# Kernel optimization log

Measured on AMD Instinct MI355X. Metric: run time of the kernel, lower is better.

## Reference

```python
import jax, jax.numpy as jnp
import numpy as np

N = 100000      # nodes
F_IN = 500      # input features
HEADS = 8
HID = 8         # per-head hidden channels
NC = 16         # num classes
E = 1600000     # edges (avg degree 16)


def setup_inputs() -> dict:
    key = jax.random.key(0)
    ks = jax.random.split(key, 12)
    s = 0.1
    return {
        "x": jax.random.normal(ks[0], (N, F_IN), jnp.float32),
        "edge_index": jax.random.randint(ks[1], (2, E), 0, N, dtype=jnp.int64),
        "W1": jax.random.normal(ks[2], (F_IN, HEADS * HID), jnp.float32) * s,
        "a1_src": jax.random.normal(ks[3], (HEADS, HID), jnp.float32) * s,
        "a1_dst": jax.random.normal(ks[4], (HEADS, HID), jnp.float32) * s,
        "b1": jnp.zeros((HEADS * HID,), jnp.float32),
        "W2": jax.random.normal(ks[5], (HEADS * HID, NC), jnp.float32) * s,
        "a2_src": jax.random.normal(ks[6], (1, NC), jnp.float32) * s,
        "a2_dst": jax.random.normal(ks[7], (1, NC), jnp.float32) * s,
        "b2": jnp.zeros((NC,), jnp.float32),
        "Wg": jax.random.normal(ks[8], (NC, NC), jnp.float32) * s,
        "bg": jnp.zeros((NC,), jnp.float32),
    }


def _gat_layer(x, src, dst, W, a_src, a_dst, b, heads, ch):
    # PyG GATConv (eval mode): per-edge additive attention + scatter softmax.
    n = x.shape[0]
    h = (x @ W).reshape(n, heads, ch)                       # [N,H,C]
    al_s = jnp.einsum('nhc,hc->nh', h, a_src)               # [N,H]
    al_d = jnp.einsum('nhc,hc->nh', h, a_dst)
    e = jax.nn.leaky_relu(al_s[src] + al_d[dst], 0.2)       # [Etot,H]
    e_max = jax.ops.segment_max(e, dst, num_segments=n)     # stable softmax per dst
    ex = jnp.exp(e - e_max[dst])
    denom = jax.ops.segment_sum(ex, dst, num_segments=n)
    alpha = ex / (denom[dst] + 1e-16)                       # [Etot,H]
    out = jax.ops.segment_sum(alpha[:, :, None] * h[src], dst, num_segments=n)
    return out.reshape(n, heads * ch) + b


def _gcn_layer(x, src, dst, W, b):
    n = x.shape[0]
    deg = jax.ops.segment_sum(jnp.ones_like(dst, x.dtype), dst, num_segments=n)
    dinv = jnp.where(deg > 0, jax.lax.rsqrt(deg), 0.0)
    norm = dinv[src] * dinv[dst]                            # [Etot]
    xw = x @ W
    return jax.ops.segment_sum(norm[:, None] * xw[src], dst, num_segments=n) + b


def reference(x, edge_index, W1, a1_src, a1_dst, b1, W2, a2_src, a2_dst, b2, Wg, bg):
    n = x.shape[0]
    loop = jnp.arange(n, dtype=edge_index.dtype)
    src = jnp.concatenate([edge_index[0], loop])            # add self-loops (PyG default)
    dst = jnp.concatenate([edge_index[1], loop])
    # GAT: dropout layers are eval-mode no-ops
    h = jax.nn.elu(_gat_layer(x, src, dst, W1, a1_src, a1_dst, b1, HEADS, HID))
    h = _gat_layer(h, src, dst, W2, a2_src, a2_dst, b2, 1, NC)
    h = jax.nn.relu(h)                                      # activate='relu'
    return _gcn_layer(h, src, dst, Wg, bg)
```

## Files before the change

kernel.cpp:

```cpp
#include <hip/hip_runtime.h>
#include <hip/hip_bf16.h>
#include <math.h>

#define NNODES 100000
#define F_IN   500
#define KPAD   512
#define HEADS  8
#define HID    8
#define NC     16

typedef __attribute__((ext_vector_type(8))) short bf16x8;
typedef __attribute__((ext_vector_type(4))) float f32x4;
typedef __attribute__((ext_vector_type(8))) unsigned short u16x8;

__device__ inline unsigned short f2bf_rne(float f) {
    unsigned u = __float_as_uint(f);
    u += 0x7FFF + ((u >> 16) & 1);
    return (unsigned short)(u >> 16);
}
__device__ inline float bf2f(unsigned short h) {
    return __uint_as_float(((unsigned)h) << 16);
}

__global__ void zero_int_kernel(int* __restrict__ p, int n) {
    int i = blockIdx.x * blockDim.x + threadIdx.x;
    if (i < n) p[i] = 0;
}

__global__ void deg_kernel(const int* __restrict__ ei_dst, int* __restrict__ deg,
                           int E, int N) {
    int e = blockIdx.x * blockDim.x + threadIdx.x;
    int tot = E + N;
    if (e >= tot) return;
    int d = (e < E) ? ei_dst[e] : (e - E);
    atomicAdd(&deg[d], 1);
}

__global__ void scan1_kernel(const int* __restrict__ deg, int* __restrict__ bsum, int n) {
    __shared__ int s[256];
    int i = blockIdx.x * 256 + threadIdx.x;
    s[threadIdx.x] = (i < n) ? deg[i] : 0;
    __syncthreads();
    for (int off = 128; off > 0; off >>= 1) {
        if (threadIdx.x < off) s[threadIdx.x] += s[threadIdx.x + off];
        __syncthreads();
    }
    if (threadIdx.x == 0) bsum[blockIdx.x] = s[0];
}

__global__ void scan2_kernel(const int* __restrict__ bsum, int* __restrict__ bexcl, int nb) {
    __shared__ int s[512];
    int t = threadIdx.x;
    int orig = (t < nb) ? bsum[t] : 0;
    s[t] = orig;
    __syncthreads();
    for (int off = 1; off < 512; off <<= 1) {
        int v = (t >= off) ? s[t - off] : 0;
        __syncthreads();
        s[t] += v;
        __syncthreads();
    }
    if (t < nb) bexcl[t] = s[t] - orig;
}

__global__ void scan3_kernel(const int* __restrict__ deg, const int* __restrict__ bexcl,
                             int* __restrict__ rowptr, int n) {
    __shared__ int s[256];
    int t = threadIdx.x;
    int i = blockIdx.x * 256 + t;
    int v = (i < n) ? deg[i] : 0;
    s[t] = v;
    __syncthreads();
    for (int off = 1; off < 256; off <<= 1) {
        int u = (t >= off) ? s[t - off] : 0;
        __syncthreads();
        s[t] += u;
        __syncthreads();
    }
    if (i < n) rowptr[i + 1] = bexcl[blockIdx.x] + s[t];
    if (i == 0) rowptr[0] = 0;
}

__global__ void fill_kernel(const int* __restrict__ ei_src, const int* __restrict__ ei_dst,
                            const int* __restrict__ rowptr, int* __restrict__ cursor,
                            int* __restrict__ col, int E, int N) {
    int e = blockIdx.x * blockDim.x + threadIdx.x;
    int tot = E + N;
    if (e >= tot) return;
    int s, d;
    if (e < E) { s = ei_src[e]; d = ei_dst[e]; }
    else       { s = e - E;     d = s; }
    int pos = atomicAdd(&cursor[d], 1);
    col[rowptr[d] + pos] = s;
}

__global__ void transposeW1_kernel(const float* __restrict__ W, float* __restrict__ Wt) {
    int i = blockIdx.x * blockDim.x + threadIdx.x;
    if (i >= 64 * KPAD) return;
    int c = i >> 9;
    int k = i & (KPAD - 1);
    Wt[i] = (k < F_IN) ? W[k * 64 + c] : 0.f;
}

#define BM  128
#define BK  32
#define LDT 40

__global__ __launch_bounds__(256) void gemm1_mfma_kernel(
        const float* __restrict__ x, const float* __restrict__ Wt,
        float* __restrict__ h, int n) {
    __shared__ unsigned short sAh[BM * LDT];
    __shared__ unsigned short sAl[BM * LDT];
    __shared__ unsigned short sBh[64 * LDT];
    __shared__ unsigned short sBl[64 * LDT];

    int t = threadIdx.x;
    int wave = t >> 6, lane = t & 63;
    int l15 = lane & 15, kgrp = lane >> 4;
    int row0 = blockIdx.x * BM;
    int wrow0 = wave * 32;

    int ar = t >> 1;
    int ak = (t & 1) * 16;
    int bc = t >> 2;
    int bk = (t & 3) * 8;

    f32x4 acc[2][4];
#pragma unroll
    for (int m = 0; m < 2; ++m)
#pragma unroll
        for (int nn = 0; nn < 4; ++nn)
            acc[m][nn] = (f32x4){0.f, 0.f, 0.f, 0.f};

    const int gr = row0 + ar;

    for (int k0 = 0; k0 < KPAD; k0 += BK) {
        float av[16];
        if (gr < n) {
            if (k0 + BK <= F_IN) {
                const float4* p = (const float4*)(x + (size_t)gr * F_IN + k0 + ak);
                float4 q0 = p[0], q1 = p[1], q2 = p[2], q3 = p[3];
                av[0]=q0.x; av[1]=q0.y; av[2]=q0.z; av[3]=q0.w;
                av[4]=q1.x; av[5]=q1.y; av[6]=q1.z; av[7]=q1.w;
                av[8]=q2.x; av[9]=q2.y; av[10]=q2.z; av[11]=q2.w;
                av[12]=q3.x; av[13]=q3.y; av[14]=q3.z; av[15]=q3.w;
            } else {
#pragma unroll
                for (int j = 0; j < 16; ++j) {
                    int kk = k0 + ak + j;
                    av[j] = (kk < F_IN) ? x[(size_t)gr * F_IN + kk] : 0.f;
                }
            }
        } else {
#pragma unroll
            for (int j = 0; j < 16; ++j) av[j] = 0.f;
        }
        u16x8 ah0, ah1, al0, al1;
#pragma unroll
        for (int j = 0; j < 8; ++j) {
            unsigned short hi = f2bf_rne(av[j]);
            ah0[j] = hi;
            al0[j] = f2bf_rne(av[j] - bf2f(hi));
        }
#pragma unroll
        for (int j = 0; j < 8; ++j) {
            unsigned short hi = f2bf_rne(av[8 + j]);
            ah1[j] = hi;
            al1[j] = f2bf_rne(av[8 + j] - bf2f(hi));
        }
        *(u16x8*)&sAh[ar * LDT + ak]     = ah0;
        *(u16x8*)&sAh[ar * LDT + ak + 8] = ah1;
        *(u16x8*)&sAl[ar * LDT + ak]     = al0;
        *(u16x8*)&sAl[ar * LDT + ak + 8] = al1;

        const float4* bp = (const float4*)(Wt + (size_t)bc * KPAD + k0 + bk);
        float4 w0 = bp[0], w1 = bp[1];
        float bv[8] = {w0.x, w0.y, w0.z, w0.w, w1.x, w1.y, w1.z, w1.w};
        u16x8 bh, bl;
#pragma unroll
        for (int j = 0; j < 8; ++j) {
            unsigned short hi = f2bf_rne(bv[j]);
            bh[j] = hi;
            bl[j] = f2bf_rne(bv[j] - bf2f(hi));
        }
        *(u16x8*)&sBh[bc * LDT + bk] = bh;
        *(u16x8*)&sBl[bc * LDT + bk] = bl;

        __syncthreads();

        bf16x8 aH[2], aL[2], bH[4], bL[4];
#pragma unroll
        for (int m = 0; m < 2; ++m) {
            int r = wrow0 + m * 16 + l15;
            aH[m] = *(const bf16x8*)&sAh[r * LDT + kgrp * 8];
            aL[m] = *(const bf16x8*)&sAl[r * LDT + kgrp * 8];
        }
#pragma unroll
        for (int nn = 0; nn < 4; ++nn) {
            int c = nn * 16 + l15;
            bH[nn] = *(const bf16x8*)&sBh[c * LDT + kgrp * 8];
            bL[nn] = *(const bf16x8*)&sBl[c * LDT + kgrp * 8];
        }
#pragma unroll
        for (int m = 0; m < 2; ++m)
#pragma unroll
            for (int nn = 0; nn < 4; ++nn) {
                acc[m][nn] = __builtin_amdgcn_mfma_f32_16x16x32_bf16(aH[m], bH[nn], acc[m][nn], 0, 0, 0);
                acc[m][nn] = __builtin_amdgcn_mfma_f32_16x16x32_bf16(aH[m], bL[nn], acc[m][nn], 0, 0, 0);
                acc[m][nn] = __builtin_amdgcn_mfma_f32_16x16x32_bf16(aL[m], bH[nn], acc[m][nn], 0, 0, 0);
            }
        __syncthreads();
    }

#pragma unroll
    for (int m = 0; m < 2; ++m) {
#pragma unroll
        for (int nn = 0; nn < 4; ++nn) {
#pragma unroll
            for (int r = 0; r < 4; ++r) {
                int row = row0 + wrow0 + m * 16 + kgrp * 4 + r;
                if (row < n)
                    h[(size_t)row * 64 + nn * 16 + l15] = acc[m][nn][r];
            }
        }
    }
}

__global__ void proj_al1_kernel(const float* __restrict__ h, const float* __restrict__ a1s,
                                const float* __restrict__ a1d, float* __restrict__ als,
                                float* __restrict__ ald, int n) {
    int nid = blockIdx.x * blockDim.x + threadIdx.x;
    if (nid >= n) return;
    const float* hp = h + (size_t)nid * 64;
#pragma unroll
    for (int hd = 0; hd < 8; ++hd) {
        float s = 0.f, d = 0.f;
#pragma unroll
        for (int c = 0; c < 8; ++c) {
            float hv = hp[hd * 8 + c];
            s += hv * a1s[hd * 8 + c];
            d += hv * a1d[hd * 8 + c];
        }
        als[nid * 8 + hd] = s;
        ald[nid * 8 + hd] = d;
    }
}

__global__ void gat1_edge_kernel(const int* __restrict__ rowptr, const int* __restrict__ col,
                                 const float* __restrict__ als, const float* __restrict__ ald,
                                 const float* __restrict__ h, const float* __restrict__ b1,
                                 float* __restrict__ out1, int n) {
    int tid = blockIdx.x * blockDim.x + threadIdx.x;
    int dst = tid >> 3, hd = tid & 7;
    if (dst >= n) return;
    int beg = rowptr[dst], end = rowptr[dst + 1];
    float ad = ald[dst * 8 + hd];
    float acc[8] = {};
    float den = 0.f;
    for (int j = beg; j < end; ++j) {
        int s = col[j];
        float e = als[s * 8 + hd] + ad;
        e = e > 0.f ? e : 0.2f * e;
        float w = expf(e);
        den += w;
        const float4* hp = reinterpret_cast<const float4*>(h + (size_t)s * 64 + hd * 8);
        float4 v0 = hp[0], v1 = hp[1];
        acc[0] += w * v0.x; acc[1] += w * v0.y; acc[2] += w * v0.z; acc[3] += w * v0.w;
        acc[4] += w * v1.x; acc[5] += w * v1.y; acc[6] += w * v1.z; acc[7] += w * v1.w;
    }
    float inv = 1.f / (den + 1e-16f);
#pragma unroll
    for (int c = 0; c < 8; ++c) {
        float v = acc[c] * inv + b1[hd * 8 + c];
        v = (v > 0.f) ? v : expm1f(v);
        out1[(size_t)dst * 64 + hd * 8 + c] = v;
    }
}

__global__ void proj2_kernel(const float* __restrict__ out1, const float* __restrict__ W2,
                             const float* __restrict__ a2s, const float* __restrict__ a2d,
                             float* __restrict__ h2, float* __restrict__ al2s,
                             float* __restrict__ al2d, int n) {
    int nid = blockIdx.x * blockDim.x + threadIdx.x;
    if (nid >= n) return;
    const float* op = out1 + (size_t)nid * 64;
    float acc[16] = {};
#pragma unroll 8
    for (int k = 0; k < 64; ++k) {
        float o = op[k];
#pragma unroll
        for (int c = 0; c < 16; ++c) acc[c] += o * W2[k * 16 + c];
    }
    float s = 0.f, d = 0.f;
#pragma unroll
    for (int c = 0; c < 16; ++c) {
        s += acc[c] * a2s[c];
        d += acc[c] * a2d[c];
        h2[(size_t)nid * 16 + c] = acc[c];
    }
    al2s[nid] = s;
    al2d[nid] = d;
}

__global__ void gat2_edge_kernel(const int* __restrict__ rowptr, const int* __restrict__ col,
                                 const float* __restrict__ al2s, const float* __restrict__ al2d,
                                 const float* __restrict__ h2, const float* __restrict__ b2,
                                 const float* __restrict__ Wg, float* __restrict__ xw,
                                 float* __restrict__ dinv, int n) {
    int dst = blockIdx.x * blockDim.x + threadIdx.x;
    if (dst >= n) return;
    int beg = rowptr[dst], end = rowptr[dst + 1];
    float ad = al2d[dst];
    float acc[16] = {};
    float den = 0.f;
    for (int j = beg; j < end; ++j) {
        int s = col[j];
        float e = al2s[s] + ad;
        e = e > 0.f ? e : 0.2f * e;
        float w = expf(e);
        den += w;
        const float4* hp = reinterpret_cast<const float4*>(h2 + (size_t)s * 16);
        float4 v0 = hp[0], v1 = hp[1], v2 = hp[2], v3 = hp[3];
        acc[0]  += w * v0.x; acc[1]  += w * v0.y; acc[2]  += w * v0.z; acc[3]  += w * v0.w;
        acc[4]  += w * v1.x; acc[5]  += w * v1.y; acc[6]  += w * v1.z; acc[7]  += w * v1.w;
        acc[8]  += w * v2.x; acc[9]  += w * v2.y; acc[10] += w * v2.z; acc[11] += w * v2.w;
        acc[12] += w * v3.x; acc[13] += w * v3.y; acc[14] += w * v3.z; acc[15] += w * v3.w;
    }
    float inv = 1.f / (den + 1e-16f);
    float r[16];
#pragma unroll
    for (int c = 0; c < 16; ++c) {
        float v = acc[c] * inv + b2[c];
        r[c] = (v > 0.f) ? v : 0.f;
    }
#pragma unroll
    for (int cp = 0; cp < 16; ++cp) {
        float s2 = 0.f;
#pragma unroll
        for (int c = 0; c < 16; ++c) s2 += r[c] * Wg[c * 16 + cp];
        xw[(size_t)dst * 16 + cp] = s2;
    }
    dinv[dst] = 1.f / sqrtf((float)(end - beg));
}

__global__ void gcn_kernel(const int* __restrict__ rowptr, const int* __restrict__ col,
                           const float* __restrict__ xw, const float* __restrict__ dinv,
                           const float* __restrict__ bg, float* __restrict__ out, int n) {
    int dst = blockIdx.x * blockDim.x + threadIdx.x;
    if (dst >= n) return;
    int beg = rowptr[dst], end = rowptr[dst + 1];
    float di = dinv[dst];
    float acc[16] = {};
    for (int j = beg; j < end; ++j) {
        int s = col[j];
        float nm = dinv[s] * di;
        const float4* xp = reinterpret_cast<const float4*>(xw + (size_t)s * 16);
        float4 v0 = xp[0], v1 = xp[1], v2 = xp[2], v3 = xp[3];
        acc[0]  += nm * v0.x; acc[1]  += nm * v0.y; acc[2]  += nm * v0.z; acc[3]  += nm * v0.w;
        acc[4]  += nm * v1.x; acc[5]  += nm * v1.y; acc[6]  += nm * v1.z; acc[7]  += nm * v1.w;
        acc[8]  += nm * v2.x; acc[9]  += nm * v2.y; acc[10] += nm * v2.z; acc[11] += nm * v2.w;
        acc[12] += nm * v3.x; acc[13] += nm * v3.y; acc[14] += nm * v3.z; acc[15] += nm * v3.w;
    }
#pragma unroll
    for (int c = 0; c < 16; ++c)
        out[(size_t)dst * 16 + c] = acc[c] + bg[c];
}

extern "C" void kernel_launch(void* const* d_in, const int* in_sizes, int n_in,
                              void* d_out, int out_size, void* d_ws, size_t ws_size,
                              hipStream_t stream) {
    const float* x    = (const float*)d_in[0];
    const int*   ei   = (const int*)d_in[1];
    const float* W1   = (const float*)d_in[2];
    const float* a1s  = (const float*)d_in[3];
    const float* a1d  = (const float*)d_in[4];
    const float* b1   = (const float*)d_in[5];
    const float* W2   = (const float*)d_in[6];
    const float* a2s  = (const float*)d_in[7];
    const float* a2d  = (const float*)d_in[8];
    const float* b2   = (const float*)d_in[9];
    const float* Wg   = (const float*)d_in[10];
    const float* bg   = (const float*)d_in[11];
    float* out = (float*)d_out;

    const int N = in_sizes[0] / F_IN;
    const int E = in_sizes[1] / 2;
    const int Etot = E + N;

    char* base = (char*)d_ws;
    size_t off = 0;
    auto alloc = [&](size_t bytes) -> char* {
        char* p = base + off;
        off = (off + bytes + 255) & ~(size_t)255;
        return p;
    };
    float* h    = (float*)alloc((size_t)N * 64 * 4);
    float* als  = (float*)alloc((size_t)N * 8 * 4);
    float* ald  = (float*)alloc((size_t)N * 8 * 4);
    float* out1 = (float*)alloc((size_t)N * 64 * 4);
    float* h2   = (float*)alloc((size_t)N * 16 * 4);
    float* al2s = (float*)alloc((size_t)N * 4);
    float* al2d = (float*)alloc((size_t)N * 4);
    float* xw   = (float*)alloc((size_t)N * 16 * 4);
    float* dinv = (float*)alloc((size_t)N * 4);
    int*   deg  = (int*)alloc((size_t)N * 4);
    int*   cur  = (int*)alloc((size_t)N * 4);
    int*   rowptr = (int*)alloc((size_t)(N + 1) * 4);
    int*   bsum = (int*)alloc(512 * 4);
    int*   bexcl= (int*)alloc(512 * 4);
    int*   col  = (int*)alloc((size_t)Etot * 4);
    float* Wt   = (float*)alloc((size_t)64 * KPAD * 4);

    const int* ei_src = ei;
    const int* ei_dst = ei + E;

    const int TB = 256;
    int nbN  = (N + TB - 1) / TB;
    int nbE  = (Etot + TB - 1) / TB;
    int nbG  = (N + BM - 1) / BM;
    int nbA  = (N * 8 + TB - 1) / TB;

    zero_int_kernel<<<nbN, TB, 0, stream>>>(deg, N);
    zero_int_kernel<<<nbN, TB, 0, stream>>>(cur, N);
    deg_kernel<<<nbE, TB, 0, stream>>>(ei_dst, deg, E, N);
    scan1_kernel<<<nbN, TB, 0, stream>>>(deg, bsum, N);
    scan2_kernel<<<1, 512, 0, stream>>>(bsum, bexcl, nbN);
    scan3_kernel<<<nbN, TB, 0, stream>>>(deg, bexcl, rowptr, N);
    fill_kernel<<<nbE, TB, 0, stream>>>(ei_src, ei_dst, rowptr, cur, col, E, N);

    transposeW1_kernel<<<(64 * KPAD + TB - 1) / TB, TB, 0, stream>>>(W1, Wt);
    gemm1_mfma_kernel<<<nbG, TB, 0, stream>>>(x, Wt, h, N);
    proj_al1_kernel<<<nbN, TB, 0, stream>>>(h, a1s, a1d, als, ald, N);
    gat1_edge_kernel<<<nbA, TB, 0, stream>>>(rowptr, col, als, ald, h, b1, out1, N);
    proj2_kernel<<<nbN, TB, 0, stream>>>(out1, W2, a2s, a2d, h2, al2s, al2d, N);
    gat2_edge_kernel<<<nbN, TB, 0, stream>>>(rowptr, col, al2s, al2d, h2, b2, Wg, xw, dinv, N);
    gcn_kernel<<<nbN, TB, 0, stream>>>(rowptr, col, xw, dinv, bg, out, N);
}
```

Measured before the change: 686.2 us.

## Record per-edge slot from degree atomics to remove second atomic pass in CSR fill

The degree-counting kernel now keeps the return value of each atomicAdd as the edge's slot within its destination row and stores it in a new per-edge pos array. The fill kernel reads that slot instead of doing a second atomic on a cursor array, so the cursor buffer and its zeroing launch are gone. Both kernels now handle four edges per thread with int4 loads, and the column writes use nontemporal stores. This trades an extra write and read of a 1.7M-int array for removing 1.7M atomics and one kernel launch.

```diff
diff --git a/kernel.cpp b/kernel.cpp
--- a/kernel.cpp
+++ b/kernel.cpp
@@ -27,13 +27,27 @@
     if (i < n) p[i] = 0;
 }
 
-__global__ void deg_kernel(const int* __restrict__ ei_dst, int* __restrict__ deg,
-                           int E, int N) {
-    int e = blockIdx.x * blockDim.x + threadIdx.x;
+__global__ void deg_pos_kernel(const int* __restrict__ ei_dst, int* __restrict__ deg,
+                               int* __restrict__ pos, int E, int N) {
     int tot = E + N;
-    if (e >= tot) return;
-    int d = (e < E) ? ei_dst[e] : (e - E);
-    atomicAdd(&deg[d], 1);
+    int i0 = (blockIdx.x * blockDim.x + threadIdx.x) * 4;
+    if (i0 >= tot) return;
+    if (i0 + 3 < E) {
+        int4 d4 = *reinterpret_cast<const int4*>(ei_dst + i0);
+        int p0 = atomicAdd(&deg[d4.x], 1);
+        int p1 = atomicAdd(&deg[d4.y], 1);
+        int p2 = atomicAdd(&deg[d4.z], 1);
+        int p3 = atomicAdd(&deg[d4.w], 1);
+        *reinterpret_cast<int4*>(pos + i0) = make_int4(p0, p1, p2, p3);
+    } else {
+#pragma unroll
+        for (int j = 0; j < 4; ++j) {
+            int e = i0 + j;
+            if (e >= tot) break;
+            int d = (e < E) ? ei_dst[e] : (e - E);
+            pos[e] = atomicAdd(&deg[d], 1);
+        }
+    }
 }
 
 __global__ void scan1_kernel(const int* __restrict__ deg, int* __restrict__ bsum, int n) {
@@ -81,17 +95,35 @@
     if (i == 0) rowptr[0] = 0;
 }
 
-__global__ void fill_kernel(const int* __restrict__ ei_src, const int* __restrict__ ei_dst,
-                            const int* __restrict__ rowptr, int* __restrict__ cursor,
-                            int* __restrict__ col, int E, int N) {
-    int e = blockIdx.x * blockDim.x + threadIdx.x;
+__global__ void fill2_kernel(const int* __restrict__ ei_src, const int* __restrict__ ei_dst,
+                             const int* __restrict__ rowptr, const int* __restrict__ pos,
+                             int* __restrict__ col, int E, int N) {
     int tot = E + N;
-    if (e >= tot) return;
-    int s, d;
-    if (e < E) { s = ei_src[e]; d = ei_dst[e]; }
-    else       { s = e - E;     d = s; }
-    int pos = atomicAdd(&cursor[d], 1);
-    col[rowptr[d] + pos] = s;
+    int i0 = (blockIdx.x * blockDim.x + threadIdx.x) * 4;
+    if (i0 >= tot) return;
+    if (i0 + 3 < E) {
+        int4 s4 = *reinterpret_cast<const int4*>(ei_src + i0);
+        int4 d4 = *reinterpret_cast<const int4*>(ei_dst + i0);
+        int4 p4 = *reinterpret_cast<const int4*>(pos + i0);
+        int o0 = rowptr[d4.x] + p4.x;
+        int o1 = rowptr[d4.y] + p4.y;
+        int o2 = rowptr[d4.z] + p4.z;
+        int o3 = rowptr[d4.w] + p4.w;
+        __builtin_nontemporal_store(s4.x, &col[o0]);
+        __builtin_nontemporal_store(s4.y, &col[o1]);
+        __builtin_nontemporal_store(s4.z, &col[o2]);
+        __builtin_nontemporal_store(s4.w, &col[o3]);
+    } else {
+#pragma unroll
+        for (int j = 0; j < 4; ++j) {
+            int e = i0 + j;
+            if (e >= tot) break;
+            int s, d;
+            if (e < E) { s = ei_src[e]; d = ei_dst[e]; }
+            else       { s = e - E;     d = s; }
+            __builtin_nontemporal_store(s, &col[rowptr[d] + pos[e]]);
+        }
+    }
 }
 
 __global__ void transposeW1_kernel(const float* __restrict__ W, float* __restrict__ Wt) {
@@ -404,11 +436,11 @@
     float* xw   = (float*)alloc((size_t)N * 16 * 4);
     float* dinv = (float*)alloc((size_t)N * 4);
     int*   deg  = (int*)alloc((size_t)N * 4);
-    int*   cur  = (int*)alloc((size_t)N * 4);
     int*   rowptr = (int*)alloc((size_t)(N + 1) * 4);
     int*   bsum = (int*)alloc(512 * 4);
     int*   bexcl= (int*)alloc(512 * 4);
     int*   col  = (int*)alloc((size_t)Etot * 4);
+    int*   pos  = (int*)alloc((size_t)Etot * 4);
     float* Wt   = (float*)alloc((size_t)64 * KPAD * 4);
 
     const int* ei_src = ei;
@@ -416,17 +448,16 @@
 
     const int TB = 256;
     int nbN  = (N + TB - 1) / TB;
-    int nbE  = (Etot + TB - 1) / TB;
+    int nbE4 = (Etot + TB * 4 - 1) / (TB * 4);
     int nbG  = (N + BM - 1) / BM;
     int nbA  = (N * 8 + TB - 1) / TB;
 
     zero_int_kernel<<<nbN, TB, 0, stream>>>(deg, N);
-    zero_int_kernel<<<nbN, TB, 0, stream>>>(cur, N);
-    deg_kernel<<<nbE, TB, 0, stream>>>(ei_dst, deg, E, N);
+    deg_pos_kernel<<<nbE4, TB, 0, stream>>>(ei_dst, deg, pos, E, N);
     scan1_kernel<<<nbN, TB, 0, stream>>>(deg, bsum, N);
     scan2_kernel<<<1, 512, 0, stream>>>(bsum, bexcl, nbN);
     scan3_kernel<<<nbN, TB, 0, stream>>>(deg, bexcl, rowptr, N);
-    fill_kernel<<<nbE, TB, 0, stream>>>(ei_src, ei_dst, rowptr, cur, col, E, N);
+    fill2_kernel<<<nbE4, TB, 0, stream>>>(ei_src, ei_dst, rowptr, pos, col, E, N);
 
     transposeW1_kernel<<<(64 * KPAD + TB - 1) / TB, TB, 0, stream>>>(W1, Wt);
     gemm1_mfma_kernel<<<nbG, TB, 0, stream>>>(x, Wt, h, N);
```

After: 665.7 us. 3.0% less time.
